# Kernel tuning notes

Measured on AMD Instinct MI355X. Metric: run time of the kernel, lower is better.

## Reference

```python
import jax, jax.numpy as jnp
import numpy as np

B, FREQ, FRAMES = 16, 513, 2048
N_FFT, HOP, WIN = 1024, 256, 1024


def _hann_periodic(n):
    # torch.hann_window(n) (periodic): 0.5 - 0.5*cos(2*pi*k/n)
    return (0.5 - 0.5 * jnp.cos(2.0 * jnp.pi * jnp.arange(n) / n)).astype(jnp.float32)


def setup_inputs() -> dict:
    key = jax.random.key(0)
    k1, k2 = jax.random.split(key)
    spec_real = jax.random.normal(k1, (B, FREQ, FRAMES), dtype=jnp.float32)
    spec_imag = jax.random.normal(k2, (B, FREQ, FRAMES), dtype=jnp.float32)
    window = _hann_periodic(WIN)
    return {
        "spec_real": spec_real,
        "spec_imag": spec_imag,
        "window": window,
        "n_fft": N_FFT,
        "hop_length": HOP,
        "win_length": WIN,
    }


def reference(spec_real, spec_imag, window, n_fft, hop_length, win_length):
    spec = spec_real + 1j * spec_imag          # [B, n_fft//2+1, n_frames] complex
    n_frames = spec.shape[-1]
    pad = (win_length - hop_length) // 2
    # irfft with torch norm='backward' == jnp default norm
    ifft = jnp.fft.irfft(spec, n=n_fft, axis=1)           # [B, n_fft, F]
    frames = (ifft * window[None, :, None]).transpose(0, 2, 1)
    out_len = (n_frames - 1) * hop_length + win_length
    # overlap-add (fold) via scatter-add
    idx = jnp.arange(n_frames)[:, None] * hop_length + jnp.arange(win_length)[None, :]
    audio = jnp.zeros((frames.shape[0], out_len), frames.dtype).at[:, idx].add(frames)
    # squared-window envelope via the same overlap-add
    env = jnp.zeros((out_len,), window.dtype).at[idx].add(
        jnp.broadcast_to(window * window, (n_frames, win_length))
    )
    audio = audio[:, pad:out_len - pad] / env[pad:out_len - pad]
    return audio[:, None, :]  # [B, 1, T]
```

## Files before the change

kernel.cpp:

```cpp
#include <hip/hip_runtime.h>


#define B_      16
#define FREQ_   513
#define FRAMES_ 2048
#define NFFT_   1024
#define HOP_    256
#define NH_     512
#define PAD_    384
#define T_OUT_  524288
#define FPW     16
#define HPW     12
#define SPW     3072
#define NCHUNK  171

#define ZSTR    521
#define XWSTR   1041
#define LDSF    16672

__device__ __forceinline__ void idft8(float* zr, float* zi) {
  const float C = 0.70710678118654752f;
  float tr, ti;
  tr = zr[0]-zr[4]; ti = zi[0]-zi[4]; zr[0]+=zr[4]; zi[0]+=zi[4]; zr[4]=tr;        zi[4]=ti;
  tr = zr[1]-zr[5]; ti = zi[1]-zi[5]; zr[1]+=zr[5]; zi[1]+=zi[5]; zr[5]=C*(tr-ti); zi[5]=C*(tr+ti);
  tr = zr[2]-zr[6]; ti = zi[2]-zi[6]; zr[2]+=zr[6]; zi[2]+=zi[6]; zr[6]=-ti;       zi[6]=tr;
  tr = zr[3]-zr[7]; ti = zi[3]-zi[7]; zr[3]+=zr[7]; zi[3]+=zi[7]; zr[7]=-C*(tr+ti); zi[7]=C*(tr-ti);
  tr = zr[0]-zr[2]; ti = zi[0]-zi[2]; zr[0]+=zr[2]; zi[0]+=zi[2]; zr[2]=tr;  zi[2]=ti;
  tr = zr[1]-zr[3]; ti = zi[1]-zi[3]; zr[1]+=zr[3]; zi[1]+=zi[3]; zr[3]=-ti; zi[3]=tr;
  tr = zr[4]-zr[6]; ti = zi[4]-zi[6]; zr[4]+=zr[6]; zi[4]+=zi[6]; zr[6]=tr;  zi[6]=ti;
  tr = zr[5]-zr[7]; ti = zi[5]-zi[7]; zr[5]+=zr[7]; zi[5]+=zi[7]; zr[7]=-ti; zi[7]=tr;
  tr = zr[0]-zr[1]; ti = zi[0]-zi[1]; zr[0]+=zr[1]; zi[0]+=zi[1]; zr[1]=tr; zi[1]=ti;
  tr = zr[2]-zr[3]; ti = zi[2]-zi[3]; zr[2]+=zr[3]; zi[2]+=zi[3]; zr[3]=tr; zi[3]=ti;
  tr = zr[4]-zr[5]; ti = zi[4]-zi[5]; zr[4]+=zr[5]; zi[4]+=zi[5]; zr[5]=tr; zi[5]=ti;
  tr = zr[6]-zr[7]; ti = zi[6]-zi[7]; zr[6]+=zr[7]; zi[6]+=zi[7]; zr[7]=tr; zi[7]=ti;
}

__global__ __launch_bounds__(256) void k_prep(const float* __restrict__ win,
                                              float2* __restrict__ tw512,
                                              float2* __restrict__ pre,
                                              float* __restrict__ invenv) {
  const int blk = blockIdx.x, t = threadIdx.x;
  if (blk == 0) {
    float s, c;
    sincosf((float)t * (6.2831853071795864769f / 512.f), &s, &c);
    tw512[t] = make_float2(c, s);
    sincosf((float)(t + 256) * (6.2831853071795864769f / 512.f), &s, &c);
    tw512[t + 256] = make_float2(c, s);
  } else if (blk == 1) {
    float s, c;
    sincosf((float)t * (3.1415926535897932385f / 512.f), &s, &c);
    pre[t] = make_float2(c, s);
    sincosf((float)(t + 256) * (3.1415926535897932385f / 512.f), &s, &c);
    pre[t + 256] = make_float2(c, s);
    if (t == 0) pre[512] = make_float2(-1.f, 0.f);
  } else {
    const int s_ = (blk - 2) * 256 + t;
    if (s_ < T_OUT_) {
      const int u  = s_ + PAD_;
      const int fh = min(FRAMES_ - 1, u >> 8);
      const int fl = (u >= NFFT_) ? (((u - NFFT_) >> 8) + 1) : 0;
      float e = 0.f;
      for (int f = fl; f <= fh; ++f) { const float w = win[u - (f << 8)]; e += w * w; }
      invenv[s_] = 1.0f / e;
    }
  }
}

__global__ __launch_bounds__(512, 4) void k_fused(
    const float* __restrict__ sre, const float* __restrict__ sim,
    const float* __restrict__ win, const float2* __restrict__ tw512,
    const float2* __restrict__ pre, const float* __restrict__ invenv,
    float* __restrict__ out) {
  __shared__ float lds[LDSF];
  float* __restrict__ ZR = lds;
  float* __restrict__ ZI = lds + 16 * ZSTR;

  const int t  = threadIdx.x;
  const int f  = t & 15;
  const int j0 = t >> 4;
  const int b   = blockIdx.x & 15;
  const int wgq = blockIdx.x >> 4;
  const int f_base = HPW * wgq - 2;
  const int s0     = SPW * wgq;
  const int fg = f_base + f;
  const bool fv = (fg >= 0) && (fg < FRAMES_);
  const int fgc = fv ? fg : 0;
  const float scale = fv ? (0.5f / 512.0f) : 0.0f;
  const size_t bbase = (size_t)b * (FREQ_ * FRAMES_);
  const float* __restrict__ srb = sre + bbase + fgc;
  const float* __restrict__ sib = sim + bbase + fgc;
  const int brev3[8] = {0, 4, 2, 6, 1, 5, 3, 7};

#pragma unroll
  for (int half = 0; half < 2; ++half) {
    const int j = j0 + 32 * half;
    float zr[8], zi[8];
#pragma unroll
    for (int m = 0; m < 8; ++m) {
      const int i  = j + (m << 6);
      const int k2 = NH_ - i;
      float xr1 = srb[(size_t)i  * FRAMES_];
      float xi1 = sib[(size_t)i  * FRAMES_];
      float xr2 = srb[(size_t)k2 * FRAMES_];
      float xi2 = sib[(size_t)k2 * FRAMES_];
      if (i == 0) { xi1 = 0.f; xi2 = 0.f; }
      const float Er = xr1 + xr2, Ei = xi1 - xi2;
      const float Dr = xr1 - xr2, Di = xi1 + xi2;
      const float2 w = pre[i];
      const float Or = w.x * Dr - w.y * Di;
      const float Oi = w.x * Di + w.y * Dr;
      zr[m] = (Er - Oi) * scale;
      zi[m] = (Ei + Or) * scale;
    }
    idft8(zr, zi);
#pragma unroll
    for (int r = 0; r < 8; ++r) {
      const int mp = brev3[r];
      const int a  = f * ZSTR + j + (mp << 6);
      if (mp == 0) { ZR[a] = zr[r]; ZI[a] = zi[r]; }
      else {
        const float2 w = tw512[j * mp];
        ZR[a] = zr[r] * w.x - zi[r] * w.y;
        ZI[a] = zr[r] * w.y + zi[r] * w.x;
      }
    }
  }
  __syncthreads();

#pragma unroll
  for (int half = 0; half < 2; ++half) {
    const int j   = j0 + 32 * half;
    const int pos = j & 7, blk = j >> 3;
    const int i0  = (blk << 6) + pos;
    float zr[8], zi[8];
#pragma unroll
    for (int m = 0; m < 8; ++m) {
      const int a = f * ZSTR + i0 + (m << 3);
      zr[m] = ZR[a]; zi[m] = ZI[a];
    }
    idft8(zr, zi);
#pragma unroll
    for (int r = 0; r < 8; ++r) {
      const int mp = brev3[r];
      const int a  = f * ZSTR + i0 + (mp << 3);
      if (mp == 0) { ZR[a] = zr[r]; ZI[a] = zi[r]; }
      else {
        const float2 w = tw512[(pos * mp) << 3];
        ZR[a] = zr[r] * w.x - zi[r] * w.y;
        ZI[a] = zr[r] * w.y + zi[r] * w.x;
      }
    }
  }
  __syncthreads();

  float yr[16], yi[16];
#pragma unroll
  for (int half = 0; half < 2; ++half) {
    const int j = j0 + 32 * half;
#pragma unroll
    for (int m = 0; m < 8; ++m) {
      const int a = f * ZSTR + (j << 3) + m;
      yr[half * 8 + m] = ZR[a];
      yi[half * 8 + m] = ZI[a];
    }
    idft8(yr + half * 8, yi + half * 8);
  }
  __syncthreads();

  float* __restrict__ XW = lds;
  const int c0 = ((j0 & 7) << 3) + (j0 >> 3);
  const float2* __restrict__ win2 = (const float2*)win;
#pragma unroll
  for (int half = 0; half < 2; ++half) {
    const int c = c0 + 4 * half;
#pragma unroll
    for (int r = 0; r < 8; ++r) {
      const int mp = brev3[r];
      const int m  = (mp << 6) + c;
      const float2 wv = win2[m];
      const int a = f * XWSTR + (m << 1);
      XW[a]     = yr[half * 8 + r] * wv.x;
      XW[a + 1] = yi[half * 8 + r] * wv.y;
    }
  }
  __syncthreads();

  float* __restrict__ outb = out + (size_t)b * T_OUT_;
#pragma unroll
  for (int r = 0; r < 3; ++r) {
    const int sl = (t + (r << 9)) << 1;
    const int s  = s0 + sl;
    if (s < T_OUT_) {
      const int u  = s + PAD_;
      const int fh = u >> 8, ob = u & 255;
      float vr = 0.f, vi = 0.f;
#pragma unroll
      for (int jj = 0; jj < 4; ++jj) {
        const int fl = fh - jj - f_base;
        const int a  = fl * XWSTR + ob + (jj << 8);
        vr += XW[a]; vi += XW[a + 1];
      }
      const float2 ie = *(const float2*)(invenv + s);
      *(float2*)(outb + s) = make_float2(vr * ie.x, vi * ie.y);
    }
  }
}

extern "C" void kernel_launch(void* const* d_in, const int* in_sizes, int n_in,
                              void* d_out, int out_size, void* d_ws, size_t ws_size,
                              hipStream_t stream) {
  const float* sre = (const float*)d_in[0];
  const float* sim = (const float*)d_in[1];
  const float* win = (const float*)d_in[2];
  float2* tw512  = (float2*)d_ws;
  float2* pre    = tw512 + 512;
  float*  invenv = (float*)((char*)d_ws + 16384);
  float*  out    = (float*)d_out;

  k_prep<<<2 + (T_OUT_ + 255) / 256, 256, 0, stream>>>(win, tw512, pre, invenv);
  k_fused<<<B_ * NCHUNK, 512, 0, stream>>>(sre, sim, win, tw512, pre, invenv, out);
}
```

Measured before the change: 222.4 us.

## Use 1024-thread blocks with interleaved complex LDS and split even/odd output buffers

Doubles the threads per block so each thread handles one radix-8 column instead of two. The FFT scratch moves from separate real and imaginary arrays to interleaved float2 entries, so each LDS access is a 64-bit load or store. The windowed output is split into even and odd planes for the overlap-add. The intent is more parallelism per block, fewer registers per thread and fewer LDS instructions. In exchange, the new strides (513) can change bank-conflict patterns, and the larger blocks may limit occupancy.

```diff
diff --git a/kernel.cpp b/kernel.cpp
--- a/kernel.cpp
+++ b/kernel.cpp
@@ -9,21 +9,20 @@
 #define NH_     512
 #define PAD_    384
 #define T_OUT_  524288
-#define FPW     16
 #define HPW     12
 #define SPW     3072
 #define NCHUNK  171
 
-#define ZSTR    521
-#define XWSTR   1041
-#define LDSF    16672
+#define ZSTR2   513
+#define XWSTR   513
+#define LDSF    16416
 
 __device__ __forceinline__ void idft8(float* zr, float* zi) {
   const float C = 0.70710678118654752f;
   float tr, ti;
-  tr = zr[0]-zr[4]; ti = zi[0]-zi[4]; zr[0]+=zr[4]; zi[0]+=zi[4]; zr[4]=tr;        zi[4]=ti;
-  tr = zr[1]-zr[5]; ti = zi[1]-zi[5]; zr[1]+=zr[5]; zi[1]+=zi[5]; zr[5]=C*(tr-ti); zi[5]=C*(tr+ti);
-  tr = zr[2]-zr[6]; ti = zi[2]-zi[6]; zr[2]+=zr[6]; zi[2]+=zi[6]; zr[6]=-ti;       zi[6]=tr;
+  tr = zr[0]-zr[4]; ti = zi[0]-zi[4]; zr[0]+=zr[4]; zi[0]+=zi[4]; zr[4]=tr;         zi[4]=ti;
+  tr = zr[1]-zr[5]; ti = zi[1]-zi[5]; zr[1]+=zr[5]; zi[1]+=zi[5]; zr[5]=C*(tr-ti);  zi[5]=C*(tr+ti);
+  tr = zr[2]-zr[6]; ti = zi[2]-zi[6]; zr[2]+=zr[6]; zi[2]+=zi[6]; zr[6]=-ti;        zi[6]=tr;
   tr = zr[3]-zr[7]; ti = zi[3]-zi[7]; zr[3]+=zr[7]; zi[3]+=zi[7]; zr[7]=-C*(tr+ti); zi[7]=C*(tr-ti);
   tr = zr[0]-zr[2]; ti = zi[0]-zi[2]; zr[0]+=zr[2]; zi[0]+=zi[2]; zr[2]=tr;  zi[2]=ti;
   tr = zr[1]-zr[3]; ti = zi[1]-zi[3]; zr[1]+=zr[3]; zi[1]+=zi[3]; zr[3]=-ti; zi[3]=tr;
@@ -66,18 +65,17 @@
   }
 }
 
-__global__ __launch_bounds__(512, 4) void k_fused(
+__global__ __launch_bounds__(1024, 8) void k_fused(
     const float* __restrict__ sre, const float* __restrict__ sim,
     const float* __restrict__ win, const float2* __restrict__ tw512,
     const float2* __restrict__ pre, const float* __restrict__ invenv,
     float* __restrict__ out) {
-  __shared__ float lds[LDSF];
-  float* __restrict__ ZR = lds;
-  float* __restrict__ ZI = lds + 16 * ZSTR;
-
-  const int t  = threadIdx.x;
-  const int f  = t & 15;
-  const int j0 = t >> 4;
+  __shared__ __align__(16) float lds[LDSF];
+  float2* __restrict__ Z2 = (float2*)lds;
+
+  const int t = threadIdx.x;
+  const int f = t & 15;
+  const int j = t >> 4;
   const int b   = blockIdx.x & 15;
   const int wgq = blockIdx.x >> 4;
   const int f_base = HPW * wgq - 2;
@@ -91,9 +89,7 @@
   const float* __restrict__ sib = sim + bbase + fgc;
   const int brev3[8] = {0, 4, 2, 6, 1, 5, 3, 7};
 
-#pragma unroll
-  for (int half = 0; half < 2; ++half) {
-    const int j = j0 + 32 * half;
+  {
     float zr[8], zi[8];
 #pragma unroll
     for (int m = 0; m < 8; ++m) {
@@ -113,95 +109,92 @@
       zi[m] = (Ei + Or) * scale;
     }
     idft8(zr, zi);
+    float2* __restrict__ zrow = Z2 + f * ZSTR2 + j;
 #pragma unroll
     for (int r = 0; r < 8; ++r) {
       const int mp = brev3[r];
-      const int a  = f * ZSTR + j + (mp << 6);
-      if (mp == 0) { ZR[a] = zr[r]; ZI[a] = zi[r]; }
+      if (mp == 0) zrow[0] = make_float2(zr[r], zi[r]);
       else {
         const float2 w = tw512[j * mp];
-        ZR[a] = zr[r] * w.x - zi[r] * w.y;
-        ZI[a] = zr[r] * w.y + zi[r] * w.x;
+        zrow[mp << 6] = make_float2(zr[r] * w.x - zi[r] * w.y,
+                                    zr[r] * w.y + zi[r] * w.x);
       }
     }
   }
   __syncthreads();
 
-#pragma unroll
-  for (int half = 0; half < 2; ++half) {
-    const int j   = j0 + 32 * half;
+  {
     const int pos = j & 7, blk = j >> 3;
-    const int i0  = (blk << 6) + pos;
+    float2* __restrict__ zrow = Z2 + f * ZSTR2 + (blk << 6) + pos;
     float zr[8], zi[8];
 #pragma unroll
     for (int m = 0; m < 8; ++m) {
-      const int a = f * ZSTR + i0 + (m << 3);
-      zr[m] = ZR[a]; zi[m] = ZI[a];
+      const float2 v = zrow[m << 3];
+      zr[m] = v.x; zi[m] = v.y;
     }
     idft8(zr, zi);
 #pragma unroll
     for (int r = 0; r < 8; ++r) {
       const int mp = brev3[r];
-      const int a  = f * ZSTR + i0 + (mp << 3);
-      if (mp == 0) { ZR[a] = zr[r]; ZI[a] = zi[r]; }
+      if (mp == 0) zrow[0] = make_float2(zr[r], zi[r]);
       else {
         const float2 w = tw512[(pos * mp) << 3];
-        ZR[a] = zr[r] * w.x - zi[r] * w.y;
-        ZI[a] = zr[r] * w.y + zi[r] * w.x;
+        zrow[mp << 3] = make_float2(zr[r] * w.x - zi[r] * w.y,
+                                    zr[r] * w.y + zi[r] * w.x);
       }
     }
   }
   __syncthreads();
 
-  float yr[16], yi[16];
-#pragma unroll
-  for (int half = 0; half < 2; ++half) {
-    const int j = j0 + 32 * half;
+  float yr[8], yi[8];
+  {
+    const float2* __restrict__ zrow = Z2 + f * ZSTR2 + (j << 3);
 #pragma unroll
     for (int m = 0; m < 8; ++m) {
-      const int a = f * ZSTR + (j << 3) + m;
-      yr[half * 8 + m] = ZR[a];
-      yi[half * 8 + m] = ZI[a];
-    }
-    idft8(yr + half * 8, yi + half * 8);
-  }
-  __syncthreads();
-
-  float* __restrict__ XW = lds;
-  const int c0 = ((j0 & 7) << 3) + (j0 >> 3);
-  const float2* __restrict__ win2 = (const float2*)win;
-#pragma unroll
-  for (int half = 0; half < 2; ++half) {
-    const int c = c0 + 4 * half;
+      const float2 v = zrow[m];
+      yr[m] = v.x; yi[m] = v.y;
+    }
+  }
+  idft8(yr, yi);
+  __syncthreads();
+
+  float* __restrict__ XWe = lds;
+  float* __restrict__ XWo = lds + 16 * XWSTR;
+  {
+    const int c = ((j & 7) << 3) + (j >> 3);
+    const float2* __restrict__ win2 = (const float2*)win;
+    float* __restrict__ er = XWe + f * XWSTR + c;
+    float* __restrict__ od = XWo + f * XWSTR + c;
 #pragma unroll
     for (int r = 0; r < 8; ++r) {
       const int mp = brev3[r];
-      const int m  = (mp << 6) + c;
-      const float2 wv = win2[m];
-      const int a = f * XWSTR + (m << 1);
-      XW[a]     = yr[half * 8 + r] * wv.x;
-      XW[a + 1] = yi[half * 8 + r] * wv.y;
+      const float2 wv = win2[(mp << 6) + c];
+      er[mp << 6] = yr[r] * wv.x;
+      od[mp << 6] = yi[r] * wv.y;
     }
   }
   __syncthreads();
 
   float* __restrict__ outb = out + (size_t)b * T_OUT_;
 #pragma unroll
-  for (int r = 0; r < 3; ++r) {
-    const int sl = (t + (r << 9)) << 1;
-    const int s  = s0 + sl;
-    if (s < T_OUT_) {
-      const int u  = s + PAD_;
-      const int fh = u >> 8, ob = u & 255;
-      float vr = 0.f, vi = 0.f;
-#pragma unroll
-      for (int jj = 0; jj < 4; ++jj) {
-        const int fl = fh - jj - f_base;
-        const int a  = fl * XWSTR + ob + (jj << 8);
-        vr += XW[a]; vi += XW[a + 1];
+  for (int rr = 0; rr < 2; ++rr) {
+    const int idx = t + (rr << 10);
+    if (idx < 1536) {
+      const int s = s0 + (idx << 1);
+      if (s < T_OUT_) {
+        const int u   = s + PAD_;
+        const int fh  = u >> 8;
+        const int me0 = (u & 255) >> 1;
+        float vr = 0.f, vi = 0.f;
+#pragma unroll
+        for (int jj = 0; jj < 4; ++jj) {
+          const int fl = fh - jj - f_base;
+          const int a  = fl * XWSTR + me0 + (jj << 7);
+          vr += XWe[a]; vi += XWo[a];
+        }
+        const float2 ie = *(const float2*)(invenv + s);
+        *(float2*)(outb + s) = make_float2(vr * ie.x, vi * ie.y);
       }
-      const float2 ie = *(const float2*)(invenv + s);
-      *(float2*)(outb + s) = make_float2(vr * ie.x, vi * ie.y);
     }
   }
 }
@@ -218,5 +211,5 @@
   float*  out    = (float*)d_out;
 
   k_prep<<<2 + (T_OUT_ + 255) / 256, 256, 0, stream>>>(win, tw512, pre, invenv);
-  k_fused<<<B_ * NCHUNK, 512, 0, stream>>>(sre, sim, win, tw512, pre, invenv, out);
-}
+  k_fused<<<B_ * NCHUNK, 1024, 0, stream>>>(sre, sim, win, tw512, pre, invenv, out);
+}
```

New measurement: 221.9 us. About the same (-0.3%).
